# Performance work log

Measured on AMD Instinct MI355X. Metric: run time of the kernel, lower is better.

## Reference

```python
import jax, jax.numpy as jnp
import numpy as np

B, S, C, HD = 1, 2048, 2048, 128
H = C // HD  # 16 heads
EPS = float(jnp.finfo(jnp.float32).eps)  # torch nn.RMSNorm default eps


def setup_inputs() -> dict:
    key = jax.random.key(0)
    ks = jax.random.split(key, 10)
    std = 1.0 / np.sqrt(C)
    return {
        "x": jax.random.normal(ks[0], (B, S, C), jnp.float32),
        "rope": jax.random.normal(ks[1], (1, S, 1, HD // 2, 2, 2), jnp.float32),
        "wq": jax.random.normal(ks[2], (C, C), jnp.float32) * std,
        "bq": jax.random.normal(ks[3], (C,), jnp.float32) * 0.01,
        "wk": jax.random.normal(ks[4], (C, C), jnp.float32) * std,
        "bk": jax.random.normal(ks[5], (C,), jnp.float32) * 0.01,
        "wv": jax.random.normal(ks[6], (C, C), jnp.float32) * std,
        "bv": jax.random.normal(ks[7], (C,), jnp.float32) * 0.01,
        "q_norm_w": jnp.ones((HD,), jnp.float32),
        "k_norm_w": jnp.ones((HD,), jnp.float32),
        "wo": jax.random.normal(ks[8], (C, C), jnp.float32) * std,
        "bo": jax.random.normal(ks[9], (C,), jnp.float32) * 0.01,
    }


def _rmsnorm(x, w):
    # x: [..., HD]
    ms = jnp.mean(x * x, axis=-1, keepdims=True)
    return x * jax.lax.rsqrt(ms + EPS) * w


def _apply_rotary(x, rope):
    # x: [B,S,H,HD]; rope: [1,S,1,HD//2,2,2]
    shp = x.shape
    x_ = x.reshape(*shp[:-1], -1, 1, 2)          # [B,S,H,HD/2,1,2]
    out = (rope * x_).sum(axis=-1)               # [B,S,H,HD/2,2]
    return out.reshape(shp)


def reference(x, rope, wq, bq, wk, bk, wv, bv, q_norm_w, k_norm_w, wo, bo):
    q = x @ wq.T + bq
    k = x @ wk.T + bk
    v = x @ wv.T + bv
    q = q.reshape(B, S, H, HD)
    k = k.reshape(B, S, H, HD)
    v = v.reshape(B, S, H, HD)
    q = _rmsnorm(q, q_norm_w)
    k = _rmsnorm(k, k_norm_w)
    q = _apply_rotary(q, rope)
    k = _apply_rotary(k, rope)
    scale = 1.0 / np.sqrt(HD)
    scores = jnp.einsum("bqhd,bkhd->bhqk", q, k) * scale  # [B,H,S,S]
    attn = jax.nn.softmax(scores, axis=-1)
    out = jnp.einsum("bhqk,bkhd->bqhd", attn, v).reshape(B, S, C)
    return out @ wo.T + bo
```

## Files before the change

kernel.cpp:

```cpp
#include <hip/hip_runtime.h>
#include <stdint.h>

#define GLOBAL_AS __attribute__((address_space(1)))
#define LDS_AS    __attribute__((address_space(3)))

typedef unsigned short u16;
typedef __attribute__((ext_vector_type(8))) __bf16 bf16x8;
typedef __attribute__((ext_vector_type(4))) float   f32x4;
typedef __attribute__((ext_vector_type(2))) float   f32x2;
typedef __attribute__((ext_vector_type(4))) u16     u16x4;

#if __has_builtin(__builtin_amdgcn_exp2f)
#define EXP2(x) __builtin_amdgcn_exp2f(x)
#else
#define EXP2(x) __exp2f(x)
#endif

static __device__ __forceinline__ float bf2f(u16 u) {
    union { uint32_t i; float f; } c; c.i = ((uint32_t)u) << 16; return c.f;
}
static __device__ __forceinline__ u16 f2bf(float f) {
    union { float f; uint32_t i; } c; c.f = f;
    uint32_t r = c.i + 0x7fffu + ((c.i >> 16) & 1u);
    return (u16)(r >> 16);
}
static __device__ __forceinline__ u16 f2bf_fast(float f) {
    union { float f; uint32_t i; } c; c.f = f;
    return (u16)((c.i + 0x8000u) >> 16);
}
static __device__ __forceinline__ void gl_lds16(const void* g, void* l) {
    __builtin_amdgcn_global_load_lds((GLOBAL_AS const uint32_t*)g,
                                     (LDS_AS uint32_t*)l, 16, 0, 0);
}
static __device__ __forceinline__ f32x4 mfma16(bf16x8 a, bf16x8 b, f32x4 c) {
    return __builtin_amdgcn_mfma_f32_16x16x32_bf16(a, b, c, 0, 0, 0);
}

__global__ __launch_bounds__(256) void cast5(
    const float* __restrict__ s0, const float* __restrict__ s1,
    const float* __restrict__ s2, const float* __restrict__ s3,
    const float* __restrict__ s4,
    u16* __restrict__ d0, u16* __restrict__ d1, u16* __restrict__ d2,
    u16* __restrict__ d3, u16* __restrict__ d4)
{
    const float* s; u16* d;
    switch (blockIdx.y) {
        case 0: s = s0; d = d0; break;
        case 1: s = s1; d = d1; break;
        case 2: s = s2; d = d2; break;
        case 3: s = s3; d = d3; break;
        default: s = s4; d = d4; break;
    }
    int i = (blockIdx.x * 256 + threadIdx.x) * 8;
    f32x4 v0 = *(const f32x4*)&s[i];
    f32x4 v1 = *(const f32x4*)&s[i + 4];
    u16x4 u0 = { f2bf(v0[0]), f2bf(v0[1]), f2bf(v0[2]), f2bf(v0[3]) };
    u16x4 u1 = { f2bf(v1[0]), f2bf(v1[1]), f2bf(v1[2]), f2bf(v1[3]) };
    *(u16x4*)&d[i] = u0;
    *(u16x4*)&d[i + 4] = u1;
}

__global__ __launch_bounds__(512, 2) void gemm_qkv7(
    const u16* __restrict__ x,
    const u16* __restrict__ wq, const u16* __restrict__ wk, const u16* __restrict__ wv,
    const float* __restrict__ bq, const float* __restrict__ bk, const float* __restrict__ bv,
    u16* __restrict__ q, u16* __restrict__ k, u16* __restrict__ vt)
{
    __shared__ u16 SL[4][16384];
    const int tid = threadIdx.x, l = tid & 63, w = tid >> 6;
    const int wm = w >> 2, wn = w & 3;
    const int lr = l & 15, lg = l >> 4;
    const int lg2 = lg ^ ((lr >> 1) & 3);
    const int bid = blockIdx.x;
    const int j = bid >> 3;
    const int bn = (bid & 7) * 4 + (j & 3);
    const int bm = j >> 2;

    const u16* Ab = x + (size_t)(bm * 256) * 2048;

    const int uA0 = tid,       rA0 = uA0 >> 2, cA0 = (uA0 & 3) ^ ((rA0 >> 1) & 3);
    const int uA1 = 512 + tid, rA1 = uA1 >> 2, cA1 = (uA1 & 3) ^ ((rA1 >> 1) & 3);
    const u16* apA0 = Ab + (size_t)rA0 * 2048 + cA0 * 8;
    const u16* apA1 = Ab + (size_t)rA1 * 2048 + cA1 * 8;
    const int ub0 = tid;
    int ub1 = 512 + tid; if (ub1 > 767) ub1 = 767;
    const int rB0 = ub0 >> 2, cB0 = (ub0 & 3) ^ ((rB0 >> 1) & 3);
    const int rB1 = ub1 >> 2, cB1 = (ub1 & 3) ^ ((rB1 >> 1) & 3);
    const int gr0 = bn * 192 + rB0, gr1 = bn * 192 + rB1;
    const u16* base0 = gr0 < 2048 ? wq : (gr0 < 4096 ? wk : wv);
    const u16* base1 = gr1 < 2048 ? wq : (gr1 < 4096 ? wk : wv);
    const u16* bpB0 = base0 + (size_t)(gr0 & 2047) * 2048 + cB0 * 8;
    const u16* bpB1 = base1 + (size_t)(gr1 & 2047) * 2048 + cB1 * 8;
    const int dA0 = uA0 * 8, dA1 = uA1 * 8;
    const int dB0 = (1024 + tid) * 8, dB1 = (1536 + tid) * 8;

    auto stageA = [&](u16* slot) {
        gl_lds16(apA0, slot + dA0);
        gl_lds16(apA1, slot + dA1);
        apA0 += 32; apA1 += 32;
    };
    auto stageB = [&](u16* slot) {
        gl_lds16(bpB0, slot + dB0);
        gl_lds16(bpB1, slot + dB1);
        bpB0 += 32; bpB1 += 32;
    };

    f32x4 acc[8][3];
#pragma unroll
    for (int mi = 0; mi < 8; ++mi)
#pragma unroll
        for (int nj = 0; nj < 3; ++nj) acc[mi][nj] = (f32x4){0.f, 0.f, 0.f, 0.f};

    stageA((u16*)SL[0]); stageB((u16*)SL[0]);
    stageA((u16*)SL[1]); stageB((u16*)SL[1]);
    stageA((u16*)SL[2]); stageB((u16*)SL[2]);

    const int ar = wm * 128 + lr;
    const int br = wn * 48 + lr;

    auto iter_body = [&](const u16* As0, const u16* As1, u16* sl3, u16* sl4) {
        const u16* Bs0 = As0 + 8192;
        const u16* Bs1 = As1 + 8192;

        asm volatile("s_waitcnt vmcnt(4)" ::: "memory");
        __builtin_amdgcn_s_barrier();
        __builtin_amdgcn_sched_barrier(0);

        bf16x8 b0[3], alo0[4], ahi0[4], b1[3], alo1[4], ahi1[4];

        stageA(sl3);
#pragma unroll
        for (int nj = 0; nj < 3; ++nj)
            b0[nj] = *(const bf16x8*)&Bs0[(br + nj * 16) * 32 + lg2 * 8];
#pragma unroll
        for (int mi = 0; mi < 4; ++mi)
            alo0[mi] = *(const bf16x8*)&As0[(ar + mi * 16) * 32 + lg2 * 8];
#pragma unroll
        for (int mi = 0; mi < 4; ++mi)
            ahi0[mi] = *(const bf16x8*)&As0[(ar + (4 + mi) * 16) * 32 + lg2 * 8];
        __builtin_amdgcn_s_setprio(1);
#pragma unroll
        for (int mi = 0; mi < 4; ++mi)
#pragma unroll
            for (int nj = 0; nj < 3; ++nj)
                acc[mi][nj] = mfma16(alo0[mi], b0[nj], acc[mi][nj]);
        __builtin_amdgcn_s_setprio(0);

        stageB(sl3);
#pragma unroll
        for (int nj = 0; nj < 3; ++nj)
            b1[nj] = *(const bf16x8*)&Bs1[(br + nj * 16) * 32 + lg2 * 8];
#pragma unroll
        for (int mi = 0; mi < 4; ++mi)
            alo1[mi] = *(const bf16x8*)&As1[(ar + mi * 16) * 32 + lg2 * 8];
        __builtin_amdgcn_s_setprio(1);
#pragma unroll
        for (int mi = 0; mi < 4; ++mi)
#pragma unroll
            for (int nj = 0; nj < 3; ++nj)
                acc[4 + mi][nj] = mfma16(ahi0[mi], b0[nj], acc[4 + mi][nj]);
        __builtin_amdgcn_s_setprio(0);

        __builtin_amdgcn_sched_barrier(0);
        __builtin_amdgcn_s_barrier();
        __builtin_amdgcn_sched_barrier(0);

        stageA(sl4);
#pragma unroll
        for (int mi = 0; mi < 4; ++mi)
            ahi1[mi] = *(const bf16x8*)&As1[(ar + (4 + mi) * 16) * 32 + lg2 * 8];
        __builtin_amdgcn_s_setprio(1);
#pragma unroll
        for (int mi = 0; mi < 4; ++mi)
#pragma unroll
            for (int nj = 0; nj < 3; ++nj)
                acc[mi][nj] = mfma16(alo1[mi], b1[nj], acc[mi][nj]);
        __builtin_amdgcn_s_setprio(0);

        stageB(sl4);
        __builtin_amdgcn_s_setprio(1);
#pragma unroll
        for (int mi = 0; mi < 4; ++mi)
#pragma unroll
            for (int nj = 0; nj < 3; ++nj)
                acc[4 + mi][nj] = mfma16(ahi1[mi], b1[nj], acc[4 + mi][nj]);
        __builtin_amdgcn_s_setprio(0);
    };

#pragma unroll 1
    for (int it2 = 0; it2 < 16; ++it2) {
        iter_body((const u16*)SL[0], (const u16*)SL[1], (u16*)SL[3], (u16*)SL[0]);
        iter_body((const u16*)SL[2], (const u16*)SL[3], (u16*)SL[1], (u16*)SL[2]);
    }
    asm volatile("s_waitcnt vmcnt(0)" ::: "memory");

#pragma unroll
    for (int mi = 0; mi < 8; ++mi) {
        int row0 = bm * 256 + wm * 128 + mi * 16 + lg * 4;
#pragma unroll
        for (int nj = 0; nj < 3; ++nj) {
            int col = bn * 192 + wn * 48 + nj * 16 + lr;
            int cs = (col >> 11), cc = col & 2047;
            const float* bp = cs == 0 ? bq : (cs == 1 ? bk : bv);
            float bs = bp[cc];
            if (cs == 2) {
                u16x4 pk = { f2bf(acc[mi][nj][0] + bs), f2bf(acc[mi][nj][1] + bs),
                             f2bf(acc[mi][nj][2] + bs), f2bf(acc[mi][nj][3] + bs) };
                *(u16x4*)&vt[(size_t)cc * 2048 + row0] = pk;
            } else {
                u16* C = cs == 0 ? q : k;
#pragma unroll
                for (int reg = 0; reg < 4; ++reg)
                    C[(size_t)(row0 + reg) * 2048 + cc] = f2bf(acc[mi][nj][reg] + bs);
            }
        }
    }
}

__global__ __launch_bounds__(512, 2) void gemm_out5(
    const u16* __restrict__ a, const u16* __restrict__ wo,
    const float* __restrict__ bo, float* __restrict__ out)
{
    __shared__ u16 SL[4][8192];
    const int tid = threadIdx.x, l = tid & 63, w = tid >> 6;
    const int wm = w >> 2, wn = w & 3;
    const int lr = l & 15, lg = l >> 4;
    const int lg2 = lg ^ ((lr >> 1) & 3);
    const int bid = blockIdx.x;
    const int xcd = bid & 7, j = bid >> 3;
    const int bm = xcd * 2 + (j & 1), bn = j >> 1;

    const u16* Ab = a  + (size_t)(bm * 128) * 2048;
    const u16* Bb = wo + (size_t)(bn * 128) * 2048;

    const int r0 = tid >> 2, c0 = (tid & 3) ^ ((r0 >> 1) & 3);
    const u16* apA = Ab + (size_t)r0 * 2048 + c0 * 8;
    const u16* bpB = Bb + (size_t)r0 * 2048 + c0 * 8;
    const int dA = tid * 8, dB = (512 + tid) * 8;

    auto stage = [&](u16* slot) {
        gl_lds16(apA, slot + dA);
        gl_lds16(bpB, slot + dB);
        apA += 32; bpB += 32;
    };

    f32x4 acc[4][2];
#pragma unroll
    for (int mi = 0; mi < 4; ++mi)
#pragma unroll
        for (int nj = 0; nj < 2; ++nj) acc[mi][nj] = (f32x4){0.f, 0.f, 0.f, 0.f};

    stage((u16*)SL[0]); stage((u16*)SL[1]); stage((u16*)SL[2]);

    auto ob = [&](const u16* As, u16* sln) {
        const u16* Bs = As + 4096;
        asm volatile("s_waitcnt vmcnt(4)" ::: "memory");
        __builtin_amdgcn_s_barrier();
        __builtin_amdgcn_sched_barrier(0);

        stage(sln);

        bf16x8 bf[2], af0[2];
#pragma unroll
        for (int nj = 0; nj < 2; ++nj)
            bf[nj] = *(const bf16x8*)&Bs[(wn * 32 + nj * 16 + lr) * 32 + lg2 * 8];
#pragma unroll
        for (int mi = 0; mi < 2; ++mi)
            af0[mi] = *(const bf16x8*)&As[(wm * 64 + mi * 16 + lr) * 32 + lg2 * 8];
        __builtin_amdgcn_s_setprio(1);
#pragma unroll
        for (int mi = 0; mi < 2; ++mi)
#pragma unroll
            for (int nj = 0; nj < 2; ++nj)
                acc[mi][nj] = mfma16(af0[mi], bf[nj], acc[mi][nj]);
        __builtin_amdgcn_s_setprio(0);
        __builtin_amdgcn_s_barrier();
        __builtin_amdgcn_sched_barrier(0);

        bf16x8 af1[2];
#pragma unroll
        for (int mi = 0; mi < 2; ++mi)
            af1[mi] = *(const bf16x8*)&As[(wm * 64 + (2 + mi) * 16 + lr) * 32 + lg2 * 8];
        __builtin_amdgcn_s_setprio(1);
#pragma unroll
        for (int mi = 0; mi < 2; ++mi)
#pragma unroll
            for (int nj = 0; nj < 2; ++nj)
                acc[2 + mi][nj] = mfma16(af1[mi], bf[nj], acc[2 + mi][nj]);
        __builtin_amdgcn_s_setprio(0);
    };

#pragma unroll 1
    for (int it4 = 0; it4 < 16; ++it4) {
        ob((const u16*)SL[0], (u16*)SL[3]);
        ob((const u16*)SL[1], (u16*)SL[0]);
        ob((const u16*)SL[2], (u16*)SL[1]);
        ob((const u16*)SL[3], (u16*)SL[2]);
    }
    asm volatile("s_waitcnt vmcnt(0)" ::: "memory");

#pragma unroll
    for (int mi = 0; mi < 4; ++mi) {
        int row0 = bm * 128 + wm * 64 + mi * 16 + lg * 4;
#pragma unroll
        for (int nj = 0; nj < 2; ++nj) {
            int col = bn * 128 + wn * 32 + nj * 16 + lr;
            float bs = bo[col];
#pragma unroll
            for (int reg = 0; reg < 4; ++reg)
                out[(size_t)(row0 + reg) * 2048 + col] = acc[mi][nj][reg] + bs;
        }
    }
}

__global__ __launch_bounds__(256) void norm_rope(
    const u16* __restrict__ qb, const u16* __restrict__ kb,
    const float* __restrict__ rope, const float* __restrict__ qw, const float* __restrict__ kw,
    u16* __restrict__ qh, u16* __restrict__ kh)
{
    const int tid = threadIdx.x, l = tid & 63, w = tid >> 6;
    const int rowid = blockIdx.x * 4 + w;
    const int h = rowid & 15, s = rowid >> 4;
    const size_t gbase = (size_t)s * 2048 + h * 128 + 2 * l;

    uint32_t qu = *(const uint32_t*)&qb[gbase];
    uint32_t ku = *(const uint32_t*)&kb[gbase];
    float q0 = bf2f((u16)qu), q1 = bf2f((u16)(qu >> 16));
    float k0 = bf2f((u16)ku), k1 = bf2f((u16)(ku >> 16));

    float sq = q0 * q0 + q1 * q1;
    float sk = k0 * k0 + k1 * k1;
#pragma unroll
    for (int m = 1; m < 64; m <<= 1) {
        sq += __shfl_xor(sq, m);
        sk += __shfl_xor(sk, m);
    }
    const float EPS = 1.1920928955078125e-07f;
    const float SCALE = 0.08838834764831845f * 1.4426950408889634f;
    float rq = rsqrtf(sq * (1.f / 128.f) + EPS) * SCALE;
    float rk = rsqrtf(sk * (1.f / 128.f) + EPS);

    f32x2 wq2 = *(const f32x2*)&qw[2 * l];
    f32x2 wk2 = *(const f32x2*)&kw[2 * l];
    float qn0 = q0 * rq * wq2[0], qn1 = q1 * rq * wq2[1];
    float kn0 = k0 * rk * wk2[0], kn1 = k1 * rk * wk2[1];

    f32x4 rr = *(const f32x4*)&rope[(size_t)s * 256 + l * 4];
    float qo0 = rr[0] * qn0 + rr[1] * qn1;
    float qo1 = rr[2] * qn0 + rr[3] * qn1;
    float ko0 = rr[0] * kn0 + rr[1] * kn1;
    float ko1 = rr[2] * kn0 + rr[3] * kn1;

    const size_t obase = ((size_t)h * 2048 + s) * 128 + 2 * l;
    *(uint32_t*)&qh[obase] = (uint32_t)f2bf(qo0) | ((uint32_t)f2bf(qo1) << 16);
    *(uint32_t*)&kh[obase] = (uint32_t)f2bf(ko0) | ((uint32_t)f2bf(ko1) << 16);
}

__global__ __launch_bounds__(256, 2) void attn(
    const u16* __restrict__ qh, const u16* __restrict__ kh,
    const u16* __restrict__ vt, u16* __restrict__ Opb, float* __restrict__ Lp)
{
    __shared__ u16 Ks[64 * 128];
    __shared__ u16 Vs[128 * 64];
    __shared__ u16 Ps[4][32 * 68];
    const int tid = threadIdx.x, l = tid & 63, w = tid >> 6;
    const int h = blockIdx.z, half = blockIdx.y;
    const int q0 = blockIdx.x * 128 + w * 32;
    const int lr = l & 15, lg = l >> 4;
    const float SHIFT = -17.312340490667562f;

    const u16* Kh = kh + (size_t)h * 2048 * 128;
    const u16* Vh = vt + (size_t)h * 128 * 2048;
    const int kvbase = half * 1024;

    bf16x8 qf[2][4];
#pragma unroll
    for (int am = 0; am < 2; ++am)
#pragma unroll
        for (int kk = 0; kk < 4; ++kk)
            qf[am][kk] = *(const bf16x8*)
                &qh[((size_t)h * 2048 + q0 + am * 16 + lr) * 128 + kk * 32 + lg * 8];

    bf16x8 onesf;
#pragma unroll
    for (int j = 0; j < 8; ++j) {
        union { u16 u; __bf16 b; } cb; cb.u = 0x3F80;
        onesf[j] = cb.b;
    }

    f32x4 o[2][8];
#pragma unroll
    for (int am = 0; am < 2; ++am)
#pragma unroll
        for (int dj = 0; dj < 8; ++dj) o[am][dj] = (f32x4){0.f, 0.f, 0.f, 0.f};
    f32x4 ol[2] = { (f32x4){0.f, 0.f, 0.f, 0.f}, (f32x4){0.f, 0.f, 0.f, 0.f} };

#pragma unroll 1
    for (int t = 0; t < 16; ++t) {
        const int kv0 = kvbase + t * 64;
        __syncthreads();
#pragma unroll
        for (int r = 0; r < 4; ++r) {
            int c = w * 4 + r;
            {
                int row = c * 4 + (l >> 4);
                int u = (l & 15) ^ (row & 7);
                gl_lds16(Kh + (size_t)(kv0 + row) * 128 + u * 8, &Ks[c * 512 + l * 8]);
            }
            {
                int row = c * 8 + (l >> 3);
                int u = (l & 7) ^ (row & 7);
                gl_lds16(Vh + (size_t)row * 2048 + kv0 + u * 8, &Vs[c * 512 + l * 8]);
            }
        }
        __syncthreads();

        f32x4 sc[2][4];
#pragma unroll
        for (int am = 0; am < 2; ++am)
#pragma unroll
            for (int nj = 0; nj < 4; ++nj)
                sc[am][nj] = (f32x4){SHIFT, SHIFT, SHIFT, SHIFT};
        __builtin_amdgcn_s_setprio(1);
#pragma unroll
        for (int kk = 0; kk < 4; ++kk)
#pragma unroll
            for (int nj = 0; nj < 4; ++nj) {
                int n = nj * 16 + lr;
                bf16x8 b = *(const bf16x8*)&Ks[n * 128 + ((kk * 4 + lg) ^ (n & 7)) * 8];
#pragma unroll
                for (int am = 0; am < 2; ++am)
                    sc[am][nj] = mfma16(qf[am][kk], b, sc[am][nj]);
            }
        __builtin_amdgcn_s_setprio(0);

#pragma unroll
        for (int am = 0; am < 2; ++am)
#pragma unroll
            for (int reg = 0; reg < 4; ++reg)
#pragma unroll
                for (int nj = 0; nj < 4; ++nj)
                    Ps[w][(am * 16 + lg * 4 + reg) * 68 + nj * 16 + lr] =
                        f2bf_fast(EXP2(sc[am][nj][reg]));
        asm volatile("s_waitcnt lgkmcnt(0)" ::: "memory");
        __builtin_amdgcn_sched_barrier(0);

        bf16x8 pa[2][2];
#pragma unroll
        for (int am = 0; am < 2; ++am)
#pragma unroll
            for (int kk2 = 0; kk2 < 2; ++kk2) {
                union { u16x4 h4[2]; bf16x8 v8; } cvt;
                cvt.h4[0] = *(const u16x4*)&Ps[w][(am * 16 + lr) * 68 + kk2 * 32 + lg * 8];
                cvt.h4[1] = *(const u16x4*)&Ps[w][(am * 16 + lr) * 68 + kk2 * 32 + lg * 8 + 4];
                pa[am][kk2] = cvt.v8;
            }
        __builtin_amdgcn_s_setprio(1);
#pragma unroll
        for (int am = 0; am < 2; ++am)
#pragma unroll
            for (int kk2 = 0; kk2 < 2; ++kk2)
                ol[am] = mfma16(pa[am][kk2], onesf, ol[am]);
#pragma unroll
        for (int dj = 0; dj < 8; ++dj)
#pragma unroll
            for (int kk2 = 0; kk2 < 2; ++kk2) {
                int n = dj * 16 + lr;
                bf16x8 b = *(const bf16x8*)&Vs[n * 64 + ((kk2 * 4 + lg) ^ (n & 7)) * 8];
#pragma unroll
                for (int am = 0; am < 2; ++am)
                    o[am][dj] = mfma16(pa[am][kk2], b, o[am][dj]);
            }
        __builtin_amdgcn_s_setprio(0);
    }

    if (lr == 0) {
#pragma unroll
        for (int am = 0; am < 2; ++am)
#pragma unroll
            for (int reg = 0; reg < 4; ++reg)
                Lp[(half * 16 + h) * 2048 + q0 + am * 16 + lg * 4 + reg] = ol[am][reg];
    }
#pragma unroll
    for (int am = 0; am < 2; ++am)
#pragma unroll
        for (int dj = 0; dj < 8; ++dj)
#pragma unroll
            for (int reg = 0; reg < 4; ++reg)
                Opb[((size_t)(half * 2048) + q0 + am * 16 + lg * 4 + reg) * 2048 +
                    h * 128 + dj * 16 + lr] = f2bf(o[am][dj][reg]);
}

__global__ __launch_bounds__(256) void combine(
    const u16* __restrict__ Opb, const float* __restrict__ Lp, u16* __restrict__ ab)
{
    int idx = (blockIdx.x * 256 + threadIdx.x) * 4;
    int s = idx >> 11, c = idx & 2047, h = c >> 7;
    u16x4 a4 = *(const u16x4*)&Opb[(size_t)s * 2048 + c];
    u16x4 b4 = *(const u16x4*)&Opb[(size_t)(2048 + s) * 2048 + c];
    float rl = 1.0f / (Lp[h * 2048 + s] + Lp[(16 + h) * 2048 + s]);
    u16x4 u = { f2bf((bf2f(a4[0]) + bf2f(b4[0])) * rl),
                f2bf((bf2f(a4[1]) + bf2f(b4[1])) * rl),
                f2bf((bf2f(a4[2]) + bf2f(b4[2])) * rl),
                f2bf((bf2f(a4[3]) + bf2f(b4[3])) * rl) };
    *(u16x4*)&ab[idx] = u;
}

extern "C" void kernel_launch(void* const* d_in, const int* in_sizes, int n_in,
                              void* d_out, int out_size, void* d_ws, size_t ws_size,
                              hipStream_t stream)
{
    (void)in_sizes; (void)n_in; (void)out_size;
    const float* x    = (const float*)d_in[0];
    const float* rope = (const float*)d_in[1];
    const float* wq   = (const float*)d_in[2];
    const float* bq   = (const float*)d_in[3];
    const float* wk   = (const float*)d_in[4];
    const float* bk   = (const float*)d_in[5];
    const float* wv   = (const float*)d_in[6];
    const float* bv   = (const float*)d_in[7];
    const float* qw   = (const float*)d_in[8];
    const float* kw   = (const float*)d_in[9];
    const float* wo   = (const float*)d_in[10];
    const float* bo   = (const float*)d_in[11];
    float* out = (float*)d_out;

    const size_t NE = 2048ull * 2048ull;
    if (ws_size < 13 * NE * 2) return;
    u16* p = (u16*)d_ws;
    u16* xb  = p; p += NE;
    u16* wqb = p; p += NE;
    u16* wkb = p; p += NE;
    u16* wvb = p; p += NE;
    u16* wob = p; p += NE;
    u16* qb  = p; p += NE;
    u16* kb  = p; p += NE;
    u16* vb  = p; p += NE;
    u16* qhb = p; p += NE;
    u16* khb = p; p += NE;
    u16* ab  = p; p += NE;
    u16* vtb = p; p += NE;
    u16* spare = p; p += NE;
    (void)spare; (void)vb;

    u16*   Opb = xb;
    float* Lp  = (float*)qb;

    cast5<<<dim3(2048, 5), 256, 0, stream>>>(x, wq, wk, wv, wo, xb, wqb, wkb, wvb, wob);
    gemm_qkv7<<<256, 512, 0, stream>>>(xb, wqb, wkb, wvb, bq, bk, bv, qb, kb, vtb);
    norm_rope<<<8192, 256, 0, stream>>>(qb, kb, rope, qw, kw, qhb, khb);
    attn<<<dim3(16, 2, 16), 256, 0, stream>>>(qhb, khb, vtb, Opb, Lp);
    combine<<<4096, 256, 0, stream>>>(Opb, Lp, ab);
    gemm_out5<<<256, 512, 0, stream>>>(ab, wob, bo, out);
}
```

Baseline: 154.4 us.

## Switch attention to 32x32 MFMA computing S^T, keep P in registers

Rewrites the attention inner loop to use 32x32x16 bf16 MFMA, computing the transposed score tile (K as A operand, Q as B) so each lane holds a column of probabilities. P is packed to bf16 and exchanged across half-waves with lane shuffles instead of a round trip through LDS, which removes the Ps buffer and its waitcnt barrier. The row sum is accumulated with scalar adds and a shuffle rather than an extra MFMA against a ones vector. This trades LDS traffic and extra MFMAs for cross-lane shuffles and a more intricate output index mapping, where a layout mistake would give wrong results.

```diff
diff --git a/kernel.cpp b/kernel.cpp
--- a/kernel.cpp
+++ b/kernel.cpp
@@ -7,6 +7,7 @@
 typedef unsigned short u16;
 typedef __attribute__((ext_vector_type(8))) __bf16 bf16x8;
 typedef __attribute__((ext_vector_type(4))) float   f32x4;
+typedef __attribute__((ext_vector_type(16))) float  f32x16;
 typedef __attribute__((ext_vector_type(2))) float   f32x2;
 typedef __attribute__((ext_vector_type(4))) u16     u16x4;
 
@@ -34,6 +35,9 @@
 }
 static __device__ __forceinline__ f32x4 mfma16(bf16x8 a, bf16x8 b, f32x4 c) {
     return __builtin_amdgcn_mfma_f32_16x16x32_bf16(a, b, c, 0, 0, 0);
+}
+static __device__ __forceinline__ f32x16 mfma32(bf16x8 a, bf16x8 b, f32x16 c) {
+    return __builtin_amdgcn_mfma_f32_32x32x16_bf16(a, b, c, 0, 0, 0);
 }
 
 __global__ __launch_bounds__(256) void cast5(
@@ -362,38 +366,27 @@
 {
     __shared__ u16 Ks[64 * 128];
     __shared__ u16 Vs[128 * 64];
-    __shared__ u16 Ps[4][32 * 68];
     const int tid = threadIdx.x, l = tid & 63, w = tid >> 6;
     const int h = blockIdx.z, half = blockIdx.y;
     const int q0 = blockIdx.x * 128 + w * 32;
-    const int lr = l & 15, lg = l >> 4;
+    const int lo = l & 31, hi = l >> 5;
     const float SHIFT = -17.312340490667562f;
 
     const u16* Kh = kh + (size_t)h * 2048 * 128;
     const u16* Vh = vt + (size_t)h * 128 * 2048;
     const int kvbase = half * 1024;
 
-    bf16x8 qf[2][4];
-#pragma unroll
-    for (int am = 0; am < 2; ++am)
-#pragma unroll
-        for (int kk = 0; kk < 4; ++kk)
-            qf[am][kk] = *(const bf16x8*)
-                &qh[((size_t)h * 2048 + q0 + am * 16 + lr) * 128 + kk * 32 + lg * 8];
-
-    bf16x8 onesf;
-#pragma unroll
-    for (int j = 0; j < 8; ++j) {
-        union { u16 u; __bf16 b; } cb; cb.u = 0x3F80;
-        onesf[j] = cb.b;
-    }
-
-    f32x4 o[2][8];
-#pragma unroll
-    for (int am = 0; am < 2; ++am)
-#pragma unroll
-        for (int dj = 0; dj < 8; ++dj) o[am][dj] = (f32x4){0.f, 0.f, 0.f, 0.f};
-    f32x4 ol[2] = { (f32x4){0.f, 0.f, 0.f, 0.f}, (f32x4){0.f, 0.f, 0.f, 0.f} };
+    bf16x8 qf[8];
+#pragma unroll
+    for (int i = 0; i < 8; ++i)
+        qf[i] = *(const bf16x8*)&qh[((size_t)h * 2048 + q0 + lo) * 128 + i * 16 + hi * 8];
+
+    f32x16 o[4];
+#pragma unroll
+    for (int dj = 0; dj < 4; ++dj)
+#pragma unroll
+        for (int r = 0; r < 16; ++r) o[dj][r] = 0.f;
+    float lsum = 0.f;
 
 #pragma unroll 1
     for (int t = 0; t < 16; ++t) {
@@ -415,80 +408,79 @@
         }
         __syncthreads();
 
-        f32x4 sc[2][4];
-#pragma unroll
-        for (int am = 0; am < 2; ++am)
-#pragma unroll
-            for (int nj = 0; nj < 4; ++nj)
-                sc[am][nj] = (f32x4){SHIFT, SHIFT, SHIFT, SHIFT};
-        __builtin_amdgcn_s_setprio(1);
-#pragma unroll
-        for (int kk = 0; kk < 4; ++kk)
-#pragma unroll
-            for (int nj = 0; nj < 4; ++nj) {
-                int n = nj * 16 + lr;
-                bf16x8 b = *(const bf16x8*)&Ks[n * 128 + ((kk * 4 + lg) ^ (n & 7)) * 8];
-#pragma unroll
-                for (int am = 0; am < 2; ++am)
-                    sc[am][nj] = mfma16(qf[am][kk], b, sc[am][nj]);
+        f32x16 sc0, sc1;
+#pragma unroll
+        for (int r = 0; r < 16; ++r) { sc0[r] = SHIFT; sc1[r] = SHIFT; }
+        __builtin_amdgcn_s_setprio(1);
+#pragma unroll
+        for (int i = 0; i < 8; ++i) {
+            int u = ((i * 2 + hi) ^ (lo & 7)) * 8;
+            bf16x8 kA0 = *(const bf16x8*)&Ks[lo * 128 + u];
+            bf16x8 kA1 = *(const bf16x8*)&Ks[(32 + lo) * 128 + u];
+            sc0 = mfma32(kA0, qf[i], sc0);
+            sc1 = mfma32(kA1, qf[i], sc1);
+        }
+        __builtin_amdgcn_s_setprio(0);
+
+        uint32_t pa[4][4];
+        float ls = 0.f;
+#pragma unroll
+        for (int c = 0; c < 2; ++c) {
+            float pv[16];
+#pragma unroll
+            for (int r = 0; r < 16; ++r) {
+                pv[r] = EXP2(c == 0 ? sc0[r] : sc1[r]);
+                ls += pv[r];
             }
-        __builtin_amdgcn_s_setprio(0);
-
-#pragma unroll
-        for (int am = 0; am < 2; ++am)
-#pragma unroll
-            for (int reg = 0; reg < 4; ++reg)
-#pragma unroll
-                for (int nj = 0; nj < 4; ++nj)
-                    Ps[w][(am * 16 + lg * 4 + reg) * 68 + nj * 16 + lr] =
-                        f2bf_fast(EXP2(sc[am][nj][reg]));
-        asm volatile("s_waitcnt lgkmcnt(0)" ::: "memory");
-        __builtin_amdgcn_sched_barrier(0);
-
-        bf16x8 pa[2][2];
-#pragma unroll
-        for (int am = 0; am < 2; ++am)
-#pragma unroll
-            for (int kk2 = 0; kk2 < 2; ++kk2) {
-                union { u16x4 h4[2]; bf16x8 v8; } cvt;
-                cvt.h4[0] = *(const u16x4*)&Ps[w][(am * 16 + lr) * 68 + kk2 * 32 + lg * 8];
-                cvt.h4[1] = *(const u16x4*)&Ps[w][(am * 16 + lr) * 68 + kk2 * 32 + lg * 8 + 4];
-                pa[am][kk2] = cvt.v8;
+#pragma unroll
+            for (int s = 0; s < 2; ++s) {
+                uint32_t pk0a = (uint32_t)f2bf_fast(pv[(2 * s) * 4 + 0]) |
+                                ((uint32_t)f2bf_fast(pv[(2 * s) * 4 + 1]) << 16);
+                uint32_t pk0b = (uint32_t)f2bf_fast(pv[(2 * s) * 4 + 2]) |
+                                ((uint32_t)f2bf_fast(pv[(2 * s) * 4 + 3]) << 16);
+                uint32_t pk1a = (uint32_t)f2bf_fast(pv[(2 * s + 1) * 4 + 0]) |
+                                ((uint32_t)f2bf_fast(pv[(2 * s + 1) * 4 + 1]) << 16);
+                uint32_t pk1b = (uint32_t)f2bf_fast(pv[(2 * s + 1) * 4 + 2]) |
+                                ((uint32_t)f2bf_fast(pv[(2 * s + 1) * 4 + 3]) << 16);
+                uint32_t x0a = __shfl_xor(pk0a, 32), x0b = __shfl_xor(pk0b, 32);
+                uint32_t x1a = __shfl_xor(pk1a, 32), x1b = __shfl_xor(pk1b, 32);
+                int ks = c * 2 + s;
+                pa[ks][0] = hi ? x1a : pk0a;
+                pa[ks][1] = hi ? x1b : pk0b;
+                pa[ks][2] = hi ? pk1a : x0a;
+                pa[ks][3] = hi ? pk1b : x0b;
             }
-        __builtin_amdgcn_s_setprio(1);
-#pragma unroll
-        for (int am = 0; am < 2; ++am)
-#pragma unroll
-            for (int kk2 = 0; kk2 < 2; ++kk2)
-                ol[am] = mfma16(pa[am][kk2], onesf, ol[am]);
-#pragma unroll
-        for (int dj = 0; dj < 8; ++dj)
-#pragma unroll
-            for (int kk2 = 0; kk2 < 2; ++kk2) {
-                int n = dj * 16 + lr;
-                bf16x8 b = *(const bf16x8*)&Vs[n * 64 + ((kk2 * 4 + lg) ^ (n & 7)) * 8];
-#pragma unroll
-                for (int am = 0; am < 2; ++am)
-                    o[am][dj] = mfma16(pa[am][kk2], b, o[am][dj]);
+        }
+        lsum += ls;
+
+        __builtin_amdgcn_s_setprio(1);
+#pragma unroll
+        for (int dj = 0; dj < 4; ++dj) {
+            int row = dj * 32 + lo;
+#pragma unroll
+            for (int ks = 0; ks < 4; ++ks) {
+                int u = ((ks * 2 + hi) ^ (lo & 7)) * 8;
+                bf16x8 vB = *(const bf16x8*)&Vs[row * 64 + u];
+                union { uint32_t d[4]; bf16x8 v; } cv;
+                cv.d[0] = pa[ks][0]; cv.d[1] = pa[ks][1];
+                cv.d[2] = pa[ks][2]; cv.d[3] = pa[ks][3];
+                o[dj] = mfma32(cv.v, vB, o[dj]);
             }
-        __builtin_amdgcn_s_setprio(0);
-    }
-
-    if (lr == 0) {
-#pragma unroll
-        for (int am = 0; am < 2; ++am)
-#pragma unroll
-            for (int reg = 0; reg < 4; ++reg)
-                Lp[(half * 16 + h) * 2048 + q0 + am * 16 + lg * 4 + reg] = ol[am][reg];
-    }
-#pragma unroll
-    for (int am = 0; am < 2; ++am)
-#pragma unroll
-        for (int dj = 0; dj < 8; ++dj)
-#pragma unroll
-            for (int reg = 0; reg < 4; ++reg)
-                Opb[((size_t)(half * 2048) + q0 + am * 16 + lg * 4 + reg) * 2048 +
-                    h * 128 + dj * 16 + lr] = f2bf(o[am][dj][reg]);
+        }
+        __builtin_amdgcn_s_setprio(0);
+    }
+
+    lsum += __shfl_xor(lsum, 32);
+    if (hi == 0)
+        Lp[(half * 16 + h) * 2048 + q0 + lo] = lsum;
+#pragma unroll
+    for (int dj = 0; dj < 4; ++dj)
+#pragma unroll
+        for (int r = 0; r < 16; ++r) {
+            int qq = q0 + (r & 3) + 8 * (r >> 2) + 4 * hi;
+            Opb[((size_t)(half * 2048) + qq) * 2048 + h * 128 + dj * 32 + lo] =
+                f2bf(o[dj][r]);
+        }
 }
 
 __global__ __launch_bounds__(256) void combine(
```

After: 155.4 us. Within noise of the previous version (+0.6%).
